# Kernel optimization log

Hardware: AMD Instinct MI355X
Metric: run time of the kernel (lower is better)

The kernel has to match this reference:

```python
import jax, jax.numpy as jnp
import numpy as np
from jax import lax

B, DIM, F, H, W = 2, 256, 4, 16, 16
HEADS, DIM_HEAD, GROUPS = 8, 64, 4
INNER = HEADS * DIM_HEAD            # 512
OFF_DIMS = INNER // GROUPS          # 128
CPB_DIM = DIM // 4                  # 64
DS = (2, 2, 2)                      # downsample_factor
OFFSET_SCALE = (2.0, 2.0, 2.0)


def norm_coords(coords, sizes):
    # coords: (..., 3) in (f, h, w) index units -> normalized to [-1, 1]
    s = jnp.array([max(sizes[0] - 1, 1), max(sizes[1] - 1, 1), max(sizes[2] - 1, 1)], dtype=coords.dtype)
    return 2.0 * coords / s - 1.0


def grid_sample_3d(vol, grid):
    # Faithful to F.grid_sample(..., mode='bilinear', padding_mode='zeros', align_corners=False)
    # vol: (N, C, D, H, W); grid: (N, P, 3) with last dim (x, y, z) -> (W, H, D) axes
    N, C, D, Hh, Ww = vol.shape
    P = grid.shape[1]
    ix = ((grid[..., 0] + 1.0) * Ww - 1.0) * 0.5
    iy = ((grid[..., 1] + 1.0) * Hh - 1.0) * 0.5
    iz = ((grid[..., 2] + 1.0) * D - 1.0) * 0.5
    x0, y0, z0 = jnp.floor(ix), jnp.floor(iy), jnp.floor(iz)
    tx, ty, tz = ix - x0, iy - y0, iz - z0
    vol_flat = vol.reshape(N, C, D * Hh * Ww)
    out = jnp.zeros((N, C, P), vol.dtype)
    for dz in (0, 1):
        for dy in (0, 1):
            for dx in (0, 1):
                xc, yc, zc = x0 + dx, y0 + dy, z0 + dz
                wgt = (jnp.where(dx, tx, 1.0 - tx) * jnp.where(dy, ty, 1.0 - ty) * jnp.where(dz, tz, 1.0 - tz))
                valid = ((xc >= 0) & (xc < Ww) & (yc >= 0) & (yc < Hh) & (zc >= 0) & (zc < D))
                xi = jnp.clip(xc, 0, Ww - 1).astype(jnp.int32)
                yi = jnp.clip(yc, 0, Hh - 1).astype(jnp.int32)
                zi = jnp.clip(zc, 0, D - 1).astype(jnp.int32)
                idx = (zi * Hh + yi) * Ww + xi                      # (N, P)
                vals = jnp.take_along_axis(vol_flat, jnp.broadcast_to(idx[:, None, :], (N, C, P)), axis=2)
                out = out + vals * (wgt * valid)[:, None, :]
    return out


def setup_inputs():
    key = jax.random.key(0)
    ks = jax.random.split(key, 16)
    r = lambda i, shape: jax.random.normal(ks[i], shape, dtype=jnp.float32) * 0.05
    return {
        'x': jax.random.normal(ks[0], (B, DIM, F, H, W), dtype=jnp.float32),
        'wq': r(1, (GROUPS, OFF_DIMS, DIM // GROUPS)),
        'wk': r(2, (GROUPS, OFF_DIMS, DIM // GROUPS)),
        'wv': r(3, (GROUPS, OFF_DIMS, DIM // GROUPS)),
        'off_dw_w': r(4, (OFF_DIMS, 1, 4, 4, 4)),
        'off_dw_b': r(5, (OFF_DIMS,)),
        'off_pw_w': r(6, (3, OFF_DIMS)),
        'cpb_w0': r(7, (3, CPB_DIM)),
        'cpb_b0': r(8, (CPB_DIM,)),
        'cpb_w1': r(9, (CPB_DIM, CPB_DIM)),
        'cpb_b1': r(10, (CPB_DIM,)),
        'cpb_w2': r(11, (CPB_DIM, HEADS // GROUPS)),
        'cpb_b2': r(12, (HEADS // GROUPS,)),
        'wo': r(13, (DIM, INNER)),
        'bo': r(14, (DIM,)),
    }


def reference(x, wq, wk, wv, off_dw_w, off_dw_b, off_pw_w, cpb_w0, cpb_b0, cpb_w1, cpb_b1, cpb_w2, cpb_b2, wo, bo):
    b = x.shape[0]
    f, h, w = x.shape[-3:]
    Pq = f * h * w
    scale = DIM_HEAD ** -0.5

    # grouped 1x1 conv to queries: channels are (g, d_out) ordered
    xg = x.reshape(b, GROUPS, DIM // GROUPS, Pq)
    q = jnp.einsum('bgip,goi->bgop', xg, wq)                        # (b, G, 128, Pq)

    # learned offsets: depthwise strided conv -> GELU -> 1x1 -> tanh -> scale
    gq = q.reshape(b * GROUPS, OFF_DIMS, f, h, w)
    off = lax.conv_general_dilated(gq, off_dw_w, window_strides=DS, padding=[(1, 1)] * 3,
                                   dimension_numbers=('NCDHW', 'OIDHW', 'NCDHW'),
                                   feature_group_count=OFF_DIMS)
    off = jax.nn.gelu(off + off_dw_b[None, :, None, None, None], approximate=False)
    off = jnp.einsum('ncdhw,oc->nodhw', off, off_pw_w)              # (bG, 3, fd, hd, wd)
    off = jnp.tanh(off) * jnp.array(OFFSET_SCALE, off.dtype)[None, :, None, None, None]

    fd, hd, wd = off.shape[-3:]
    Pj = fd * hd * wd
    base = jnp.stack(jnp.meshgrid(jnp.arange(fd), jnp.arange(hd), jnp.arange(wd), indexing='ij'), axis=0).astype(off.dtype)
    vgrid = base[None] + off
    vgrid_scaled = norm_coords(jnp.moveaxis(vgrid, 1, -1), (fd, hd, wd))  # (bG, fd, hd, wd, 3)
    grid_kv = vgrid_scaled.reshape(b * GROUPS, Pj, 3)

    # irregular gather of grouped features at deformed locations
    kv = grid_sample_3d(x.reshape(b * GROUPS, DIM // GROUPS, f, h, w), grid_kv)  # (bG, 64, Pj)
    kvg = kv.reshape(b, GROUPS, DIM // GROUPS, Pj)
    k = jnp.einsum('bgip,goi->bgop', kvg, wk)
    v = jnp.einsum('bgip,goi->bgop', kvg, wv)

    qh = (q * scale).reshape(b, HEADS, DIM_HEAD, Pq)
    kh = k.reshape(b, HEADS, DIM_HEAD, Pj)
    vh = v.reshape(b, HEADS, DIM_HEAD, Pj)
    sim = jnp.einsum('bhdi,bhdj->bhij', qh, kh)                     # (b, H, Pq, Pj)

    # CPB relative-position bias over (log-signed) pairwise grid differences
    baseq = jnp.stack(jnp.meshgrid(jnp.arange(f), jnp.arange(h), jnp.arange(w), indexing='ij'), axis=-1).astype(x.dtype)
    grid_q = norm_coords(baseq, (f, h, w)).reshape(Pq, 3)
    pos = grid_q[None, :, None, :] - grid_kv[:, None, :, :]         # (bG, Pq, Pj, 3)
    bias = jnp.sign(pos) * jnp.log1p(jnp.abs(pos))
    bias = jax.nn.relu(bias @ cpb_w0 + cpb_b0)
    bias = jax.nn.relu(bias @ cpb_w1 + cpb_b1)
    bias = bias @ cpb_w2 + cpb_b2                                   # (bG, Pq, Pj, H//G)
    bias = bias.reshape(b, GROUPS, Pq, Pj, HEADS // GROUPS)
    bias = jnp.transpose(bias, (0, 1, 4, 2, 3)).reshape(b, HEADS, Pq, Pj)

    attn = jax.nn.softmax(sim + bias, axis=-1)
    out = jnp.einsum('bhij,bhdj->bhdi', attn, vh).reshape(b, INNER, Pq)
    out = jnp.einsum('bcp,oc->bop', out, wo) + bo[None, :, None]
    return out.reshape(b, DIM, f, h, w)
```

## Files before the change

### kernel.cpp

```cpp
#include <hip/hip_runtime.h>
#include <hip/hip_bf16.h>
#include <hip/hip_fp16.h>
#include <math.h>

#define BB 2
#define DIMC 256
#define FF 4
#define HH 16
#define WW 16
#define GRP 4
#define CPG 64
#define ODIM 128
#define PQ 1024
#define PJ 128
#define NBG 8
#define INNERC 512

typedef _Float16 f16x8 __attribute__((ext_vector_type(8)));
typedef _Float16 f16x2 __attribute__((ext_vector_type(2)));
typedef float f32x4 __attribute__((ext_vector_type(4)));
typedef float f32x2 __attribute__((ext_vector_type(2)));

__global__ __launch_bounds__(512) void k_qdw(
    const float* __restrict__ x, const float* __restrict__ wq,
    const float* __restrict__ dww, const float* __restrict__ dwb,
    float* __restrict__ q, float* __restrict__ act) {
    __shared__ float qs[1024 * 4];
    int og = blockIdx.x & 31, bg = blockIdx.x >> 5;
    int b = bg >> 2, g = bg & 3;
    int o0 = og * 4;
    int tid = threadIdx.x;
    const float* xp = x + (size_t)(b * DIMC + g * CPG) * PQ;
    const float* wp = wq + (size_t)(g * ODIM + o0) * CPG;

    float accq[2][4] = {};
    #pragma unroll 8
    for (int i = 0; i < CPG; ++i) {
        float wv[4];
        #pragma unroll
        for (int k = 0; k < 4; ++k) wv[k] = wp[k * CPG + i];
        #pragma unroll
        for (int pi = 0; pi < 2; ++pi) {
            float xv = xp[(size_t)i * PQ + tid + pi * 512];
            #pragma unroll
            for (int k = 0; k < 4; ++k) accq[pi][k] += xv * wv[k];
        }
    }
    #pragma unroll
    for (int pi = 0; pi < 2; ++pi) {
        int p = tid + pi * 512;
        *(float4*)&qs[p * 4] = make_float4(accq[pi][0], accq[pi][1], accq[pi][2], accq[pi][3]);
        #pragma unroll
        for (int k = 0; k < 4; ++k)
            q[(size_t)(bg * ODIM + o0 + k) * PQ + p] = accq[pi][k];
    }
    __syncthreads();

    {
        int cl = tid & 3, j = tid >> 2;
        int c = o0 + cl;
        int xo = j & 7, yo = (j >> 3) & 7, zo = j >> 6;
        const float* wd = dww + c * 64;
        float acc = dwb[c];
        #pragma unroll
        for (int kz = 0; kz < 4; ++kz) {
            int z = 2 * zo - 1 + kz;
            if (z < 0 || z >= FF) continue;
            #pragma unroll
            for (int ky = 0; ky < 4; ++ky) {
                int y = 2 * yo - 1 + ky;
                if (y < 0 || y >= HH) continue;
                #pragma unroll
                for (int kx = 0; kx < 4; ++kx) {
                    int xx = 2 * xo - 1 + kx;
                    if (xx < 0 || xx >= WW) continue;
                    acc += qs[((z * HH + y) * WW + xx) * 4 + cl] * wd[(kz * 4 + ky) * 4 + kx];
                }
            }
        }
        act[((size_t)bg * PJ + j) * ODIM + c] =
            0.5f * acc * (1.0f + erff(acc * 0.70710678118654752f));
    }
}

__global__ __launch_bounds__(256) void k_kvf(
    const float* __restrict__ act, const float* __restrict__ pw,
    const float* __restrict__ x, const float* __restrict__ wk,
    const float* __restrict__ wv, float* __restrict__ gkv,
    _Float16* __restrict__ khT, _Float16* __restrict__ vhT) {
    __shared__ float red2[2][6];
    __shared__ float crd[2][3];
    __shared__ float kvs[2][64];
    int blk = blockIdx.x;
    int jt = blk & 63, bg = blk >> 6;
    int b = bg >> 2, g = bg & 3;
    int tid = threadIdx.x;
    int half = tid >> 7;
    int t = tid & 127;
    int j = jt * 2 + half;
    int wv_ = t >> 6;

    float val = act[((size_t)bg * PJ + j) * ODIM + t];
    float s0 = val * pw[t];
    float s1 = val * pw[ODIM + t];
    float s2 = val * pw[2 * ODIM + t];
    #pragma unroll
    for (int off = 32; off; off >>= 1) {
        s0 += __shfl_xor(s0, off);
        s1 += __shfl_xor(s1, off);
        s2 += __shfl_xor(s2, off);
    }
    if ((t & 63) == 0) {
        red2[half][wv_ * 3] = s0; red2[half][wv_ * 3 + 1] = s1; red2[half][wv_ * 3 + 2] = s2;
    }
    __syncthreads();
    if (t == 0) {
        s0 = red2[half][0] + red2[half][3];
        s1 = red2[half][1] + red2[half][4];
        s2 = red2[half][2] + red2[half][5];
        float xo = (float)(j & 7), yo = (float)((j >> 3) & 7), zo = (float)(j >> 6);
        float vf = zo + 2.f * tanhf(s0);
        float vh = yo + 2.f * tanhf(s1);
        float vw = xo + 2.f * tanhf(s2);
        float c0 = 2.f * vf - 1.f;
        float c1 = 2.f * vh / 7.f - 1.f;
        float c2 = 2.f * vw / 7.f - 1.f;
        crd[half][0] = c0; crd[half][1] = c1; crd[half][2] = c2;
        gkv[(bg * PJ + j) * 3 + 0] = c0;
        gkv[(bg * PJ + j) * 3 + 1] = c1;
        gkv[(bg * PJ + j) * 3 + 2] = c2;
    }
    __syncthreads();

    if (t < 64) {
        float ix = ((crd[half][0] + 1.f) * WW - 1.f) * 0.5f;
        float iy = ((crd[half][1] + 1.f) * HH - 1.f) * 0.5f;
        float iz = ((crd[half][2] + 1.f) * FF - 1.f) * 0.5f;
        float x0f = floorf(ix), y0f = floorf(iy), z0f = floorf(iz);
        float tx = ix - x0f, ty = iy - y0f, tz = iz - z0f;
        int x0 = (int)x0f, y0 = (int)y0f, z0 = (int)z0f;
        const float* vol = x + (size_t)(b * DIMC + g * CPG + t) * PQ;
        float acc = 0.f;
        #pragma unroll
        for (int dz = 0; dz < 2; ++dz) {
            int zc = z0 + dz;
            if (zc < 0 || zc >= FF) continue;
            float wz = dz ? tz : 1.f - tz;
            #pragma unroll
            for (int dy = 0; dy < 2; ++dy) {
                int yc = y0 + dy;
                if (yc < 0 || yc >= HH) continue;
                float wy = dy ? ty : 1.f - ty;
                #pragma unroll
                for (int dx = 0; dx < 2; ++dx) {
                    int xc = x0 + dx;
                    if (xc < 0 || xc >= WW) continue;
                    float wgt = wz * wy * (dx ? tx : 1.f - tx);
                    acc += vol[(zc * HH + yc) * WW + xc] * wgt;
                }
            }
        }
        kvs[half][t] = acc;
    }
    __syncthreads();

    const float* wkp = wk + (size_t)(g * ODIM + t) * CPG;
    const float* wvp = wv + (size_t)(g * ODIM + t) * CPG;
    float ak = 0.f, av = 0.f;
    #pragma unroll
    for (int i = 0; i < 64; i += 4) {
        float4 kv4 = *(const float4*)&kvs[half][i];
        float4 wk4 = *(const float4*)&wkp[i];
        float4 wv4 = *(const float4*)&wvp[i];
        ak += kv4.x * wk4.x + kv4.y * wk4.y + kv4.z * wk4.z + kv4.w * wk4.w;
        av += kv4.x * wv4.x + kv4.y * wv4.y + kv4.z * wv4.z + kv4.w * wv4.w;
    }
    {
        _Float16 khi = (_Float16)ak;
        khT[((size_t)(bg * 128 + j) * 2 + 0) * 128 + t] = khi;
        khT[((size_t)(bg * 128 + j) * 2 + 1) * 128 + t] = (_Float16)(ak - (float)khi);
        _Float16 vhi = (_Float16)av;
        vhT[((size_t)(bg * 128 + t) * 2 + 0) * 128 + j] = vhi;
        vhT[((size_t)(bg * 128 + t) * 2 + 1) * 128 + j] = (_Float16)(av - (float)vhi);
    }
}

__global__ __launch_bounds__(256) void k_cpa(
    const float* __restrict__ q, const _Float16* __restrict__ khT,
    const _Float16* __restrict__ vhT, const float* __restrict__ gkv,
    const float* __restrict__ w0, const float* __restrict__ b0,
    const float* __restrict__ w1, const float* __restrict__ b1,
    const float* __restrict__ w2, const float* __restrict__ b2,
    float* __restrict__ outh) {
    __shared__ __align__(16) float tbuf[4 * 2176];
    __shared__ __align__(16) float biasL[2 * 16 * 132];
    __shared__ float smax[64];
    __shared__ float ssum[64];

    int blk = blockIdx.x;
    int it = blk & 63, bg = blk >> 6;
    int b = bg >> 2, g = bg & 3;
    int tid = threadIdx.x;
    int w = tid >> 6, lane = tid & 63, col = lane & 15, quad = lane >> 4;

    uint4 bfr[2][4];
    #pragma unroll
    for (int kc = 0; kc < 2; ++kc)
        #pragma unroll
        for (int nt = 0; nt < 4; ++nt) {
            int n = nt * 16 + col;
            int kbase = kc * 32 + quad * 8;
            unsigned int pk[4];
            #pragma unroll
            for (int p = 0; p < 4; ++p) {
                f16x2 hv = {(_Float16)w1[(kbase + 2 * p) * 64 + n],
                            (_Float16)w1[(kbase + 2 * p + 1) * 64 + n]};
                pk[p] = *(unsigned int*)&hv;
            }
            bfr[kc][nt] = make_uint4(pk[0], pk[1], pk[2], pk[3]);
        }

    f16x2 w0a[2][4], w0b[2][4], w0c[2][4], b0h[2][4];
    #pragma unroll
    for (int kc = 0; kc < 2; ++kc) {
        int d0 = kc * 32 + quad * 8;
        #pragma unroll
        for (int pr = 0; pr < 4; ++pr) {
            w0a[kc][pr] = (f16x2){(_Float16)w0[d0 + 2 * pr], (_Float16)w0[d0 + 2 * pr + 1]};
            w0b[kc][pr] = (f16x2){(_Float16)w0[64 + d0 + 2 * pr], (_Float16)w0[64 + d0 + 2 * pr + 1]};
            w0c[kc][pr] = (f16x2){(_Float16)w0[128 + d0 + 2 * pr], (_Float16)w0[128 + d0 + 2 * pr + 1]};
            b0h[kc][pr] = (f16x2){(_Float16)b0[d0 + 2 * pr], (_Float16)b0[d0 + 2 * pr + 1]};
        }
    }
    f16x2 zero2 = {(_Float16)0.f, (_Float16)0.f};

    float g0r[8], g1r[8], g2r[8];
    #pragma unroll
    for (int mtg = 0; mtg < 8; ++mtg) {
        int jr = mtg * 16 + col;
        g0r[mtg] = gkv[(bg * PJ + jr) * 3 + 0];
        g1r[mtg] = gkv[(bg * PJ + jr) * 3 + 1];
        g2r[mtg] = gkv[(bg * PJ + jr) * 3 + 2];
    }
    float b1v[4]; f32x2 w2v[4];
    #pragma unroll
    for (int nt = 0; nt < 4; ++nt) {
        int jj = nt * 16 + col;
        b1v[nt] = b1[jj];
        w2v[nt] = *(const f32x2*)&w2[jj * 2];
    }
    f32x2 bias_b2 = *(const f32x2*)b2;
    f32x2* mytb = (f32x2*)&tbuf[w * 2176];

    #pragma unroll 1
    for (int ii = 0; ii < 4; ++ii) {
        int il = w * 4 + ii;
        int i = it * 16 + il;
        int wq_ = i & 15, hq = (i >> 4) & 15, fq = i >> 8;
        float cq0 = 2.f * fq / 3.f - 1.f;
        float cq1 = 2.f * hq / 15.f - 1.f;
        float cq2 = 2.f * wq_ / 15.f - 1.f;

        #pragma unroll 1
        for (int mh = 0; mh < 2; ++mh) {
            f16x2 t0h[4], t1h[4], t2h[4];
            #pragma unroll
            for (int mt = 0; mt < 4; ++mt) {
                int mtg = mh * 4 + mt;
                float p0 = cq0 - g0r[mtg];
                float p1 = cq1 - g1r[mtg];
                float p2 = cq2 - g2r[mtg];
                float t0 = copysignf(__logf(1.f + fabsf(p0)), p0);
                float t1 = copysignf(__logf(1.f + fabsf(p1)), p1);
                float t2 = copysignf(__logf(1.f + fabsf(p2)), p2);
                _Float16 h0 = (_Float16)t0, h1 = (_Float16)t1, h2 = (_Float16)t2;
                t0h[mt] = (f16x2){h0, h0};
                t1h[mt] = (f16x2){h1, h1};
                t2h[mt] = (f16x2){h2, h2};
            }
            f32x4 acc[4][4] = {};
            #pragma unroll
            for (int kc = 0; kc < 2; ++kc) {
                #pragma unroll
                for (int mt = 0; mt < 4; ++mt) {
                    unsigned int pk[4];
                    #pragma unroll
                    for (int pr = 0; pr < 4; ++pr) {
                        f16x2 z = b0h[kc][pr];
                        z += t0h[mt] * w0a[kc][pr];
                        z += t1h[mt] * w0b[kc][pr];
                        z += t2h[mt] * w0c[kc][pr];
                        z = __builtin_elementwise_max(z, zero2);
                        pk[pr] = *(unsigned int*)&z;
                    }
                    uint4 afu = make_uint4(pk[0], pk[1], pk[2], pk[3]);
                    f16x8 af = *(f16x8*)&afu;
                    #pragma unroll
                    for (int nt = 0; nt < 4; ++nt)
                        acc[mt][nt] = __builtin_amdgcn_mfma_f32_16x16x32_f16(
                            af, *(f16x8*)&bfr[kc][nt], acc[mt][nt], 0, 0, 0);
                }
            }
            #pragma unroll
            for (int mt = 0; mt < 4; ++mt)
                #pragma unroll
                for (int reg = 0; reg < 4; ++reg) {
                    f32x2 pp = {0.f, 0.f};
                    #pragma unroll
                    for (int nt = 0; nt < 4; ++nt) {
                        float hv = fmaxf(acc[mt][nt][reg] + b1v[nt], 0.f);
                        pp += hv * w2v[nt];
                    }
                    mytb[(mt * 16 + quad * 4 + reg) * 17 + col] = pp;
                }
            f32x2 s = bias_b2;
            {
                const f32x2* pr2 = mytb + lane * 17;
                #pragma unroll
                for (int c = 0; c < 16; ++c) s += pr2[c];
            }
            int jl = mh * 64 + lane;
            biasL[il * 132 + jl] = s.x;
            biasL[(16 + il) * 132 + jl] = s.y;
        }
    }
    __syncthreads();

    _Float16* attFh = (_Float16*)tbuf;
    _Float16* attFl = attFh + 4352;
    _Float16* qsFh  = attFh + 8704;
    _Float16* qsFl  = attFh + 10880;

    {
        int o = tid & 127, hf = tid >> 7;
        const float* qp = q + (size_t)(bg * ODIM + o) * PQ + it * 16 + hf * 8;
        float4 qa = *(const float4*)qp;
        float4 qb = *(const float4*)(qp + 4);
        float vals[8] = {qa.x, qa.y, qa.z, qa.w, qb.x, qb.y, qb.z, qb.w};
        #pragma unroll
        for (int k = 0; k < 8; ++k) {
            float v = vals[k] * 0.125f;
            _Float16 vhi = (_Float16)v;
            qsFh[(hf * 8 + k) * 136 + o] = vhi;
            qsFl[(hf * 8 + k) * 136 + o] = (_Float16)(v - (float)vhi);
        }
    }
    __syncthreads();

    int h = w >> 1, jh = w & 1;

    f16x8 aqh[2], aql[2];
    #pragma unroll
    for (int kc = 0; kc < 2; ++kc) {
        aqh[kc] = *(f16x8*)&qsFh[col * 136 + h * 64 + kc * 32 + quad * 8];
        aql[kc] = *(f16x8*)&qsFl[col * 136 + h * 64 + kc * 32 + quad * 8];
    }
    f32x4 acc[4];
    #pragma unroll
    for (int jt = 0; jt < 4; ++jt) {
        int j0 = jh * 64 + jt * 16;
        #pragma unroll
        for (int r = 0; r < 4; ++r)
            acc[jt][r] = biasL[(h * 16 + quad * 4 + r) * 132 + j0 + col];
    }
    const _Float16* kbase = khT + (size_t)(bg * 128) * 256 + h * 64 + quad * 8;
    #pragma unroll
    for (int kc = 0; kc < 2; ++kc) {
        #pragma unroll
        for (int jt = 0; jt < 4; ++jt) {
            const _Float16* kp = kbase + (size_t)(jh * 64 + jt * 16 + col) * 256 + kc * 32;
            f16x8 bh = *(const f16x8*)kp;
            f16x8 bl = *(const f16x8*)(kp + 128);
            acc[jt] = __builtin_amdgcn_mfma_f32_16x16x32_f16(aqh[kc], bh, acc[jt], 0, 0, 0);
            acc[jt] = __builtin_amdgcn_mfma_f32_16x16x32_f16(aql[kc], bh, acc[jt], 0, 0, 0);
            acc[jt] = __builtin_amdgcn_mfma_f32_16x16x32_f16(aqh[kc], bl, acc[jt], 0, 0, 0);
        }
    }

    float mrow[4];
    #pragma unroll
    for (int r = 0; r < 4; ++r) {
        float m = fmaxf(fmaxf(acc[0][r], acc[1][r]), fmaxf(acc[2][r], acc[3][r]));
        #pragma unroll
        for (int off = 1; off <= 8; off <<= 1) m = fmaxf(m, __shfl_xor(m, off));
        mrow[r] = m;
    }
    if (col == 0) {
        #pragma unroll
        for (int r = 0; r < 4; ++r) smax[(h * 2 + jh) * 16 + quad * 4 + r] = mrow[r];
    }
    __syncthreads();
    #pragma unroll
    for (int r = 0; r < 4; ++r)
        mrow[r] = fmaxf(smax[(h * 2) * 16 + quad * 4 + r],
                        smax[(h * 2 + 1) * 16 + quad * 4 + r]);

    float lrow[4] = {0.f, 0.f, 0.f, 0.f};
    #pragma unroll
    for (int jt = 0; jt < 4; ++jt) {
        int j0 = jh * 64 + jt * 16;
        #pragma unroll
        for (int r = 0; r < 4; ++r) {
            float p = __expf(acc[jt][r] - mrow[r]);
            lrow[r] += p;
            _Float16 phi = (_Float16)p;
            attFh[(h * 16 + quad * 4 + r) * 136 + j0 + col] = phi;
            attFl[(h * 16 + quad * 4 + r) * 136 + j0 + col] = (_Float16)(p - (float)phi);
        }
    }
    #pragma unroll
    for (int r = 0; r < 4; ++r) {
        float l = lrow[r];
        #pragma unroll
        for (int off = 1; off <= 8; off <<= 1) l += __shfl_xor(l, off);
        lrow[r] = l;
    }
    if (col == 0) {
        #pragma unroll
        for (int r = 0; r < 4; ++r) ssum[(h * 2 + jh) * 16 + quad * 4 + r] = lrow[r];
    }
    __syncthreads();

    f16x8 pah[4], pal[4];
    #pragma unroll
    for (int kc = 0; kc < 4; ++kc) {
        pah[kc] = *(f16x8*)&attFh[(h * 16 + col) * 136 + kc * 32 + quad * 8];
        pal[kc] = *(f16x8*)&attFl[(h * 16 + col) * 136 + kc * 32 + quad * 8];
    }
    float rinv[4];
    #pragma unroll
    for (int r = 0; r < 4; ++r)
        rinv[r] = 1.f / (ssum[(h * 2) * 16 + quad * 4 + r] +
                         ssum[(h * 2 + 1) * 16 + quad * 4 + r]);

    f32x4 oacc[2] = {};
    int chl0 = jh * 32 + col;
    #pragma unroll
    for (int kc = 0; kc < 4; ++kc) {
        #pragma unroll
        for (int nt = 0; nt < 2; ++nt) {
            int chl = chl0 + nt * 16;
            const _Float16* vp = vhT + (size_t)(bg * 128 + h * 64 + chl) * 256 + kc * 32 + quad * 8;
            f16x8 vh8 = *(const f16x8*)vp;
            f16x8 vl8 = *(const f16x8*)(vp + 128);
            oacc[nt] = __builtin_amdgcn_mfma_f32_16x16x32_f16(pah[kc], vh8, oacc[nt], 0, 0, 0);
            oacc[nt] = __builtin_amdgcn_mfma_f32_16x16x32_f16(pal[kc], vh8, oacc[nt], 0, 0, 0);
            oacc[nt] = __builtin_amdgcn_mfma_f32_16x16x32_f16(pah[kc], vl8, oacc[nt], 0, 0, 0);
        }
    }
    #pragma unroll
    for (int nt = 0; nt < 2; ++nt) {
        int chl = chl0 + nt * 16;
        #pragma unroll
        for (int r = 0; r < 4; ++r)
            outh[((size_t)(b * PQ + it * 16 + quad * 4 + r)) * INNERC + g * 128 + h * 64 + chl] =
                oacc[nt][r] * rinv[r];
    }
}

__global__ __launch_bounds__(256) void k_out(
    const float* __restrict__ outh, const float* __restrict__ wo,
    const float* __restrict__ bo, float* __restrict__ out) {
    __shared__ float At[32][68];
    __shared__ float Bt[32][36];
    int blk = blockIdx.x;
    int nt = blk & 7, mt = blk >> 3;
    int m0 = mt * 64, o0 = nt * 32;
    int tid = threadIdx.x;
    int tm = tid >> 4, tn = tid & 15;
    int mloc = tm * 4, nloc = tn * 2;

    int ra = tid >> 2, ca = (tid & 3) * 8;
    int rb = tid >> 3, cb = (tid & 7) * 4;

    float4 pa0, pa1, pb;
    {
        const float* Ap = outh + (size_t)(m0 + ra) * INNERC + ca;
        pa0 = *(const float4*)Ap;
        pa1 = *(const float4*)(Ap + 4);
        pb = *(const float4*)(wo + (size_t)(o0 + rb) * INNERC + cb);
    }

    float acc[4][2] = {};
    for (int ch = 0; ch < 16; ++ch) {
        #pragma unroll
        for (int k = 0; k < 4; ++k) {
            At[ca + k][ra] = ((const float*)&pa0)[k];
            At[ca + 4 + k][ra] = ((const float*)&pa1)[k];
            Bt[cb + k][rb] = ((const float*)&pb)[k];
        }
        __syncthreads();
        if (ch < 15) {
            int c0 = (ch + 1) * 32;
            const float* Ap = outh + (size_t)(m0 + ra) * INNERC + c0 + ca;
            pa0 = *(const float4*)Ap;
            pa1 = *(const float4*)(Ap + 4);
            pb = *(const float4*)(wo + (size_t)(o0 + rb) * INNERC + c0 + cb);
        }
        #pragma unroll
        for (int kk = 0; kk < 32; ++kk) {
            float4 a4 = *(const float4*)&At[kk][mloc];
            float2 b2 = *(const float2*)&Bt[kk][nloc];
            #pragma unroll
            for (int i = 0; i < 4; ++i) {
                float av = ((const float*)&a4)[i];
                acc[i][0] += av * b2.x;
                acc[i][1] += av * b2.y;
            }
        }
        __syncthreads();
    }

    #pragma unroll
    for (int jn = 0; jn < 2; ++jn) {
        int o = o0 + nloc + jn;
        float bv = bo[o];
        #pragma unroll
        for (int i = 0; i < 4; ++i) {
            int m = m0 + mloc + i;
            int b = m >> 10, p = m & 1023;
            out[((size_t)(b * DIMC + o)) * PQ + p] = acc[i][jn] + bv;
        }
    }
}

extern "C" void kernel_launch(void* const* d_in, const int* in_sizes, int n_in,
                              void* d_out, int out_size, void* d_ws, size_t ws_size,
                              hipStream_t stream) {
    const float* x   = (const float*)d_in[0];
    const float* wq  = (const float*)d_in[1];
    const float* wk  = (const float*)d_in[2];
    const float* wv  = (const float*)d_in[3];
    const float* dww = (const float*)d_in[4];
    const float* dwb = (const float*)d_in[5];
    const float* pw  = (const float*)d_in[6];
    const float* w0  = (const float*)d_in[7];
    const float* b0  = (const float*)d_in[8];
    const float* w1  = (const float*)d_in[9];
    const float* b1  = (const float*)d_in[10];
    const float* w2  = (const float*)d_in[11];
    const float* b2  = (const float*)d_in[12];
    const float* wo  = (const float*)d_in[13];
    const float* bo  = (const float*)d_in[14];
    float* out = (float*)d_out;

    float* ws_f  = (float*)d_ws;
    float* q     = ws_f;
    float* act   = q + 1048576;
    float* gkv   = act + 131072;
    _Float16* khT = (_Float16*)(gkv + 3072);
    _Float16* vhT = (_Float16*)(gkv + 3072 + 131072);
    float* outh  = gkv + 3072 + 262144;

    k_qdw<<<256, 512, 0, stream>>>(x, wq, dww, dwb, q, act);
    k_kvf<<<512, 256, 0, stream>>>(act, pw, x, wk, wv, gkv, khT, vhT);
    k_cpa<<<512, 256, 0, stream>>>(q, khT, vhT, gkv, w0, b0, w1, b1, w2, b2, outh);
    k_out<<<256, 256, 0, stream>>>(outh, wo, bo, out);
}
```

Measured before the change: 158.0 us.

## Use split-fp16 MFMA for output projection and double k_cpa block threads

```diff
diff --git a/kernel.cpp b/kernel.cpp
--- a/kernel.cpp
+++ b/kernel.cpp
@@ -17,6 +17,7 @@
 #define INNERC 512
 
 typedef _Float16 f16x8 __attribute__((ext_vector_type(8)));
+typedef _Float16 f16x4 __attribute__((ext_vector_type(4)));
 typedef _Float16 f16x2 __attribute__((ext_vector_type(2)));
 typedef float f32x4 __attribute__((ext_vector_type(4)));
 typedef float f32x2 __attribute__((ext_vector_type(2)));
@@ -185,17 +186,17 @@
     }
 }
 
-__global__ __launch_bounds__(256) void k_cpa(
+__global__ __launch_bounds__(512) void k_cpa(
     const float* __restrict__ q, const _Float16* __restrict__ khT,
     const _Float16* __restrict__ vhT, const float* __restrict__ gkv,
     const float* __restrict__ w0, const float* __restrict__ b0,
     const float* __restrict__ w1, const float* __restrict__ b1,
     const float* __restrict__ w2, const float* __restrict__ b2,
-    float* __restrict__ outh) {
-    __shared__ __align__(16) float tbuf[4 * 2176];
+    _Float16* __restrict__ outhH, _Float16* __restrict__ outhL) {
+    __shared__ __align__(16) float ubuf[6528];
     __shared__ __align__(16) float biasL[2 * 16 * 132];
-    __shared__ float smax[64];
-    __shared__ float ssum[64];
+    __shared__ float smax[128];
+    __shared__ float ssum[128];
 
     int blk = blockIdx.x;
     int it = blk & 63, bg = blk >> 6;
@@ -250,11 +251,11 @@
         w2v[nt] = *(const f32x2*)&w2[jj * 2];
     }
     f32x2 bias_b2 = *(const f32x2*)b2;
-    f32x2* mytb = (f32x2*)&tbuf[w * 2176];
+    f32x2* mytb = (f32x2*)&ubuf[w * 544];
 
     #pragma unroll 1
-    for (int ii = 0; ii < 4; ++ii) {
-        int il = w * 4 + ii;
+    for (int ii = 0; ii < 2; ++ii) {
+        int il = w * 2 + ii;
         int i = it * 16 + il;
         int wq_ = i & 15, hq = (i >> 4) & 15, fq = i >> 8;
         float cq0 = 2.f * fq / 3.f - 1.f;
@@ -302,7 +303,7 @@
                 }
             }
             #pragma unroll
-            for (int mt = 0; mt < 4; ++mt)
+            for (int mt = 0; mt < 4; ++mt) {
                 #pragma unroll
                 for (int reg = 0; reg < 4; ++reg) {
                     f32x2 pp = {0.f, 0.f};
@@ -311,43 +312,45 @@
                         float hv = fmaxf(acc[mt][nt][reg] + b1v[nt], 0.f);
                         pp += hv * w2v[nt];
                     }
-                    mytb[(mt * 16 + quad * 4 + reg) * 17 + col] = pp;
+                    mytb[(quad * 4 + reg) * 17 + col] = pp;
                 }
-            f32x2 s = bias_b2;
-            {
-                const f32x2* pr2 = mytb + lane * 17;
-                #pragma unroll
-                for (int c = 0; c < 16; ++c) s += pr2[c];
+                f32x2 s = mytb[col * 17 + quad * 4 + 0];
+                s += mytb[col * 17 + quad * 4 + 1];
+                s += mytb[col * 17 + quad * 4 + 2];
+                s += mytb[col * 17 + quad * 4 + 3];
+                s.x += __shfl_xor(s.x, 16); s.y += __shfl_xor(s.y, 16);
+                s.x += __shfl_xor(s.x, 32); s.y += __shfl_xor(s.y, 32);
+                if (quad == 0) {
+                    int jl = mh * 64 + mt * 16 + col;
+                    biasL[il * 132 + jl] = s.x + bias_b2.x;
+                    biasL[(16 + il) * 132 + jl] = s.y + bias_b2.y;
+                }
             }
-            int jl = mh * 64 + lane;
-            biasL[il * 132 + jl] = s.x;
-            biasL[(16 + il) * 132 + jl] = s.y;
-        }
-    }
-    __syncthreads();
-
-    _Float16* attFh = (_Float16*)tbuf;
+        }
+    }
+    __syncthreads();
+
+    _Float16* attFh = (_Float16*)ubuf;
     _Float16* attFl = attFh + 4352;
     _Float16* qsFh  = attFh + 8704;
     _Float16* qsFl  = attFh + 10880;
 
     {
         int o = tid & 127, hf = tid >> 7;
-        const float* qp = q + (size_t)(bg * ODIM + o) * PQ + it * 16 + hf * 8;
+        const float* qp = q + (size_t)(bg * ODIM + o) * PQ + it * 16 + hf * 4;
         float4 qa = *(const float4*)qp;
-        float4 qb = *(const float4*)(qp + 4);
-        float vals[8] = {qa.x, qa.y, qa.z, qa.w, qb.x, qb.y, qb.z, qb.w};
-        #pragma unroll
-        for (int k = 0; k < 8; ++k) {
-            float v = vals[k] * 0.125f;
+        float vals[4] = {qa.x, qa.y, qa.z, qa.w};
+        #pragma unroll
+        for (int k2 = 0; k2 < 4; ++k2) {
+            float v = vals[k2] * 0.125f;
             _Float16 vhi = (_Float16)v;
-            qsFh[(hf * 8 + k) * 136 + o] = vhi;
-            qsFl[(hf * 8 + k) * 136 + o] = (_Float16)(v - (float)vhi);
-        }
-    }
-    __syncthreads();
-
-    int h = w >> 1, jh = w & 1;
+            qsFh[(hf * 4 + k2) * 136 + o] = vhi;
+            qsFl[(hf * 4 + k2) * 136 + o] = (_Float16)(v - (float)vhi);
+        }
+    }
+    __syncthreads();
+
+    int h = w >> 2, p4 = w & 3;
 
     f16x8 aqh[2], aql[2];
     #pragma unroll
@@ -355,20 +358,20 @@
         aqh[kc] = *(f16x8*)&qsFh[col * 136 + h * 64 + kc * 32 + quad * 8];
         aql[kc] = *(f16x8*)&qsFl[col * 136 + h * 64 + kc * 32 + quad * 8];
     }
-    f32x4 acc[4];
-    #pragma unroll
-    for (int jt = 0; jt < 4; ++jt) {
-        int j0 = jh * 64 + jt * 16;
+    f32x4 acc[2];
+    #pragma unroll
+    for (int jt = 0; jt < 2; ++jt) {
+        int j0 = p4 * 32 + jt * 16;
         #pragma unroll
         for (int r = 0; r < 4; ++r)
             acc[jt][r] = biasL[(h * 16 + quad * 4 + r) * 132 + j0 + col];
     }
-    const _Float16* kbase = khT + (size_t)(bg * 128) * 256 + h * 64 + quad * 8;
     #pragma unroll
     for (int kc = 0; kc < 2; ++kc) {
         #pragma unroll
-        for (int jt = 0; jt < 4; ++jt) {
-            const _Float16* kp = kbase + (size_t)(jh * 64 + jt * 16 + col) * 256 + kc * 32;
+        for (int jt = 0; jt < 2; ++jt) {
+            const _Float16* kp = khT + (size_t)(bg * 128 + p4 * 32 + jt * 16 + col) * 256
+                                 + h * 64 + kc * 32 + quad * 8;
             f16x8 bh = *(const f16x8*)kp;
             f16x8 bl = *(const f16x8*)(kp + 128);
             acc[jt] = __builtin_amdgcn_mfma_f32_16x16x32_f16(aqh[kc], bh, acc[jt], 0, 0, 0);
@@ -380,25 +383,29 @@
     float mrow[4];
     #pragma unroll
     for (int r = 0; r < 4; ++r) {
-        float m = fmaxf(fmaxf(acc[0][r], acc[1][r]), fmaxf(acc[2][r], acc[3][r]));
+        float m = fmaxf(acc[0][r], acc[1][r]);
         #pragma unroll
         for (int off = 1; off <= 8; off <<= 1) m = fmaxf(m, __shfl_xor(m, off));
         mrow[r] = m;
     }
     if (col == 0) {
         #pragma unroll
-        for (int r = 0; r < 4; ++r) smax[(h * 2 + jh) * 16 + quad * 4 + r] = mrow[r];
-    }
-    __syncthreads();
-    #pragma unroll
-    for (int r = 0; r < 4; ++r)
-        mrow[r] = fmaxf(smax[(h * 2) * 16 + quad * 4 + r],
-                        smax[(h * 2 + 1) * 16 + quad * 4 + r]);
+        for (int r = 0; r < 4; ++r) smax[(h * 4 + p4) * 16 + quad * 4 + r] = mrow[r];
+    }
+    __syncthreads();
+    #pragma unroll
+    for (int r = 0; r < 4; ++r) {
+        float m = smax[(h * 4 + 0) * 16 + quad * 4 + r];
+        m = fmaxf(m, smax[(h * 4 + 1) * 16 + quad * 4 + r]);
+        m = fmaxf(m, smax[(h * 4 + 2) * 16 + quad * 4 + r]);
+        m = fmaxf(m, smax[(h * 4 + 3) * 16 + quad * 4 + r]);
+        mrow[r] = m;
+    }
 
     float lrow[4] = {0.f, 0.f, 0.f, 0.f};
     #pragma unroll
-    for (int jt = 0; jt < 4; ++jt) {
-        int j0 = jh * 64 + jt * 16;
+    for (int jt = 0; jt < 2; ++jt) {
+        int j0 = p4 * 32 + jt * 16;
         #pragma unroll
         for (int r = 0; r < 4; ++r) {
             float p = __expf(acc[jt][r] - mrow[r]);
@@ -417,7 +424,7 @@
     }
     if (col == 0) {
         #pragma unroll
-        for (int r = 0; r < 4; ++r) ssum[(h * 2 + jh) * 16 + quad * 4 + r] = lrow[r];
+        for (int r = 0; r < 4; ++r) ssum[(h * 4 + p4) * 16 + quad * 4 + r] = lrow[r];
     }
     __syncthreads();
 
@@ -430,97 +437,84 @@
     float rinv[4];
     #pragma unroll
     for (int r = 0; r < 4; ++r)
-        rinv[r] = 1.f / (ssum[(h * 2) * 16 + quad * 4 + r] +
-                         ssum[(h * 2 + 1) * 16 + quad * 4 + r]);
+        rinv[r] = 1.f / (ssum[(h * 4 + 0) * 16 + quad * 4 + r] +
+                         ssum[(h * 4 + 1) * 16 + quad * 4 + r] +
+                         ssum[(h * 4 + 2) * 16 + quad * 4 + r] +
+                         ssum[(h * 4 + 3) * 16 + quad * 4 + r]);
+
+    f32x4 oacc = {};
+    int chl = p4 * 16 + col;
+    #pragma unroll
+    for (int kc = 0; kc < 4; ++kc) {
+        const _Float16* vp = vhT + (size_t)(bg * 128 + h * 64 + chl) * 256 + kc * 32 + quad * 8;
+        f16x8 vh8 = *(const f16x8*)vp;
+        f16x8 vl8 = *(const f16x8*)(vp + 128);
+        oacc = __builtin_amdgcn_mfma_f32_16x16x32_f16(pah[kc], vh8, oacc, 0, 0, 0);
+        oacc = __builtin_amdgcn_mfma_f32_16x16x32_f16(pal[kc], vh8, oacc, 0, 0, 0);
+        oacc = __builtin_amdgcn_mfma_f32_16x16x32_f16(pah[kc], vl8, oacc, 0, 0, 0);
+    }
+    #pragma unroll
+    for (int r = 0; r < 4; ++r) {
+        float val = oacc[r] * rinv[r];
+        size_t idx = ((size_t)(b * PQ + it * 16 + quad * 4 + r)) * INNERC + g * 128 + h * 64 + chl;
+        _Float16 vhi = (_Float16)val;
+        outhH[idx] = vhi;
+        outhL[idx] = (_Float16)(val - (float)vhi);
+    }
+}
+
+__global__ __launch_bounds__(256) void k_wcvt(
+    const float* __restrict__ wo, _Float16* __restrict__ woH, _Float16* __restrict__ woL) {
+    int i = (blockIdx.x * 256 + threadIdx.x) * 4;
+    float4 v = *(const float4*)&wo[i];
+    f16x4 hh, ll;
+    hh[0] = (_Float16)v.x; ll[0] = (_Float16)(v.x - (float)hh[0]);
+    hh[1] = (_Float16)v.y; ll[1] = (_Float16)(v.y - (float)hh[1]);
+    hh[2] = (_Float16)v.z; ll[2] = (_Float16)(v.z - (float)hh[2]);
+    hh[3] = (_Float16)v.w; ll[3] = (_Float16)(v.w - (float)hh[3]);
+    *(f16x4*)&woH[i] = hh;
+    *(f16x4*)&woL[i] = ll;
+}
+
+__global__ __launch_bounds__(256) void k_out(
+    const _Float16* __restrict__ outhH, const _Float16* __restrict__ outhL,
+    const _Float16* __restrict__ woH, const _Float16* __restrict__ woL,
+    const float* __restrict__ bo, float* __restrict__ out) {
+    int blk = blockIdx.x;
+    int ntb = blk & 7, mtb = blk >> 3;
+    int tid = threadIdx.x;
+    int w = tid >> 6, lane = tid & 63, col = lane & 15, quad = lane >> 4;
+    int m0 = mtb * 64 + w * 16;
+    int o0 = ntb * 32;
+
+    const _Float16* ahb = outhH + (size_t)(m0 + col) * INNERC + quad * 8;
+    const _Float16* alb = outhL + (size_t)(m0 + col) * INNERC + quad * 8;
 
     f32x4 oacc[2] = {};
-    int chl0 = jh * 32 + col;
-    #pragma unroll
-    for (int kc = 0; kc < 4; ++kc) {
+    #pragma unroll 4
+    for (int ks = 0; ks < 16; ++ks) {
+        f16x8 ah = *(const f16x8*)(ahb + ks * 32);
+        f16x8 al = *(const f16x8*)(alb + ks * 32);
         #pragma unroll
         for (int nt = 0; nt < 2; ++nt) {
-            int chl = chl0 + nt * 16;
-            const _Float16* vp = vhT + (size_t)(bg * 128 + h * 64 + chl) * 256 + kc * 32 + quad * 8;
-            f16x8 vh8 = *(const f16x8*)vp;
-            f16x8 vl8 = *(const f16x8*)(vp + 128);
-            oacc[nt] = __builtin_amdgcn_mfma_f32_16x16x32_f16(pah[kc], vh8, oacc[nt], 0, 0, 0);
-            oacc[nt] = __builtin_amdgcn_mfma_f32_16x16x32_f16(pal[kc], vh8, oacc[nt], 0, 0, 0);
-            oacc[nt] = __builtin_amdgcn_mfma_f32_16x16x32_f16(pah[kc], vl8, oacc[nt], 0, 0, 0);
+            const _Float16* bp = woH + (size_t)(o0 + nt * 16 + col) * INNERC + ks * 32 + quad * 8;
+            const _Float16* lp = woL + (size_t)(o0 + nt * 16 + col) * INNERC + ks * 32 + quad * 8;
+            f16x8 bh = *(const f16x8*)bp;
+            f16x8 bl = *(const f16x8*)lp;
+            oacc[nt] = __builtin_amdgcn_mfma_f32_16x16x32_f16(ah, bh, oacc[nt], 0, 0, 0);
+            oacc[nt] = __builtin_amdgcn_mfma_f32_16x16x32_f16(al, bh, oacc[nt], 0, 0, 0);
+            oacc[nt] = __builtin_amdgcn_mfma_f32_16x16x32_f16(ah, bl, oacc[nt], 0, 0, 0);
         }
     }
     #pragma unroll
     for (int nt = 0; nt < 2; ++nt) {
-        int chl = chl0 + nt * 16;
-        #pragma unroll
-        for (int r = 0; r < 4; ++r)
-            outh[((size_t)(b * PQ + it * 16 + quad * 4 + r)) * INNERC + g * 128 + h * 64 + chl] =
-                oacc[nt][r] * rinv[r];
-    }
-}
-
-__global__ __launch_bounds__(256) void k_out(
-    const float* __restrict__ outh, const float* __restrict__ wo,
-    const float* __restrict__ bo, float* __restrict__ out) {
-    __shared__ float At[32][68];
-    __shared__ float Bt[32][36];
-    int blk = blockIdx.x;
-    int nt = blk & 7, mt = blk >> 3;
-    int m0 = mt * 64, o0 = nt * 32;
-    int tid = threadIdx.x;
-    int tm = tid >> 4, tn = tid & 15;
-    int mloc = tm * 4, nloc = tn * 2;
-
-    int ra = tid >> 2, ca = (tid & 3) * 8;
-    int rb = tid >> 3, cb = (tid & 7) * 4;
-
-    float4 pa0, pa1, pb;
-    {
-        const float* Ap = outh + (size_t)(m0 + ra) * INNERC + ca;
-        pa0 = *(const float4*)Ap;
-        pa1 = *(const float4*)(Ap + 4);
-        pb = *(const float4*)(wo + (size_t)(o0 + rb) * INNERC + cb);
-    }
-
-    float acc[4][2] = {};
-    for (int ch = 0; ch < 16; ++ch) {
-        #pragma unroll
-        for (int k = 0; k < 4; ++k) {
-            At[ca + k][ra] = ((const float*)&pa0)[k];
-            At[ca + 4 + k][ra] = ((const float*)&pa1)[k];
-            Bt[cb + k][rb] = ((const float*)&pb)[k];
-        }
-        __syncthreads();
-        if (ch < 15) {
-            int c0 = (ch + 1) * 32;
-            const float* Ap = outh + (size_t)(m0 + ra) * INNERC + c0 + ca;
-            pa0 = *(const float4*)Ap;
-            pa1 = *(const float4*)(Ap + 4);
-            pb = *(const float4*)(wo + (size_t)(o0 + rb) * INNERC + c0 + cb);
-        }
-        #pragma unroll
-        for (int kk = 0; kk < 32; ++kk) {
-            float4 a4 = *(const float4*)&At[kk][mloc];
-            float2 b2 = *(const float2*)&Bt[kk][nloc];
-            #pragma unroll
-            for (int i = 0; i < 4; ++i) {
-                float av = ((const float*)&a4)[i];
-                acc[i][0] += av * b2.x;
-                acc[i][1] += av * b2.y;
-            }
-        }
-        __syncthreads();
-    }
-
-    #pragma unroll
-    for (int jn = 0; jn < 2; ++jn) {
-        int o = o0 + nloc + jn;
+        int o = o0 + nt * 16 + col;
         float bv = bo[o];
-        #pragma unroll
-        for (int i = 0; i < 4; ++i) {
-            int m = m0 + mloc + i;
-            int b = m >> 10, p = m & 1023;
-            out[((size_t)(b * DIMC + o)) * PQ + p] = acc[i][jn] + bv;
-        }
+        int m = m0 + quad * 4;
+        int bb = m >> 10, p = m & 1023;
+        float4 st = make_float4(oacc[nt][0] + bv, oacc[nt][1] + bv,
+                                oacc[nt][2] + bv, oacc[nt][3] + bv);
+        *(float4*)&out[((size_t)(bb * DIMC + o)) * PQ + p] = st;
     }
 }
 
@@ -548,12 +542,16 @@
     float* q     = ws_f;
     float* act   = q + 1048576;
     float* gkv   = act + 131072;
-    _Float16* khT = (_Float16*)(gkv + 3072);
-    _Float16* vhT = (_Float16*)(gkv + 3072 + 131072);
-    float* outh  = gkv + 3072 + 262144;
-
+    _Float16* khT   = (_Float16*)(gkv + 3072);
+    _Float16* vhT   = khT + 262144;
+    _Float16* outhH = vhT + 262144;
+    _Float16* outhL = outhH + 1048576;
+    _Float16* woH   = outhL + 1048576;
+    _Float16* woL   = woH + 131072;
+
+    k_wcvt<<<128, 256, 0, stream>>>(wo, woH, woL);
     k_qdw<<<256, 512, 0, stream>>>(x, wq, dww, dwb, q, act);
     k_kvf<<<512, 256, 0, stream>>>(act, pw, x, wk, wv, gkv, khT, vhT);
-    k_cpa<<<512, 256, 0, stream>>>(q, khT, vhT, gkv, w0, b0, w1, b1, w2, b2, outh);
-    k_out<<<256, 256, 0, stream>>>(outh, wo, bo, out);
+    k_cpa<<<512, 512, 0, stream>>>(q, khT, vhT, gkv, w0, b0, w1, b1, w2, b2, outhH, outhL);
+    k_out<<<256, 256, 0, stream>>>(outhH, outhL, woH, woL, bo, out);
 }
```

Measured after the change: 164.7 us. 4.2% more time.

## Split bias MLP into its own kernel and move output projection to split-fp16 MFMA

Applied to the files above, without the earlier changes.

```diff
diff --git a/kernel.cpp b/kernel.cpp
--- a/kernel.cpp
+++ b/kernel.cpp
@@ -17,6 +17,7 @@
 #define INNERC 512
 
 typedef _Float16 f16x8 __attribute__((ext_vector_type(8)));
+typedef _Float16 f16x4 __attribute__((ext_vector_type(4)));
 typedef _Float16 f16x2 __attribute__((ext_vector_type(2)));
 typedef float f32x4 __attribute__((ext_vector_type(4)));
 typedef float f32x2 __attribute__((ext_vector_type(2)));
@@ -24,12 +25,22 @@
 __global__ __launch_bounds__(512) void k_qdw(
     const float* __restrict__ x, const float* __restrict__ wq,
     const float* __restrict__ dww, const float* __restrict__ dwb,
+    const float* __restrict__ wo, _Float16* __restrict__ woH, _Float16* __restrict__ woL,
     float* __restrict__ q, float* __restrict__ act) {
     __shared__ float qs[1024 * 4];
     int og = blockIdx.x & 31, bg = blockIdx.x >> 5;
     int b = bg >> 2, g = bg & 3;
     int o0 = og * 4;
     int tid = threadIdx.x;
+
+    {
+        int i = blockIdx.x * 512 + tid;
+        float v = wo[i];
+        _Float16 hh = (_Float16)v;
+        woH[i] = hh;
+        woL[i] = (_Float16)(v - (float)hh);
+    }
+
     const float* xp = x + (size_t)(b * DIMC + g * CPG) * PQ;
     const float* wp = wq + (size_t)(g * ODIM + o0) * CPG;
 
@@ -185,21 +196,15 @@
     }
 }
 
-__global__ __launch_bounds__(256) void k_cpa(
-    const float* __restrict__ q, const _Float16* __restrict__ khT,
-    const _Float16* __restrict__ vhT, const float* __restrict__ gkv,
+__global__ __launch_bounds__(256, 4) void k_bias(
+    const float* __restrict__ gkv,
     const float* __restrict__ w0, const float* __restrict__ b0,
     const float* __restrict__ w1, const float* __restrict__ b1,
     const float* __restrict__ w2, const float* __restrict__ b2,
-    float* __restrict__ outh) {
+    float* __restrict__ biasG) {
     __shared__ __align__(16) float tbuf[4 * 2176];
-    __shared__ __align__(16) float biasL[2 * 16 * 132];
-    __shared__ float smax[64];
-    __shared__ float ssum[64];
-
     int blk = blockIdx.x;
-    int it = blk & 63, bg = blk >> 6;
-    int b = bg >> 2, g = bg & 3;
+    int mh = blk & 1, it = (blk >> 1) & 63, bg = blk >> 7;
     int tid = threadIdx.x;
     int w = tid >> 6, lane = tid & 63, col = lane & 15, quad = lane >> 4;
 
@@ -234,13 +239,13 @@
     }
     f16x2 zero2 = {(_Float16)0.f, (_Float16)0.f};
 
-    float g0r[8], g1r[8], g2r[8];
-    #pragma unroll
-    for (int mtg = 0; mtg < 8; ++mtg) {
-        int jr = mtg * 16 + col;
-        g0r[mtg] = gkv[(bg * PJ + jr) * 3 + 0];
-        g1r[mtg] = gkv[(bg * PJ + jr) * 3 + 1];
-        g2r[mtg] = gkv[(bg * PJ + jr) * 3 + 2];
+    float g0r[4], g1r[4], g2r[4];
+    #pragma unroll
+    for (int mt = 0; mt < 4; ++mt) {
+        int jr = (mh * 4 + mt) * 16 + col;
+        g0r[mt] = gkv[(bg * PJ + jr) * 3 + 0];
+        g1r[mt] = gkv[(bg * PJ + jr) * 3 + 1];
+        g2r[mt] = gkv[(bg * PJ + jr) * 3 + 2];
     }
     float b1v[4]; f32x2 w2v[4];
     #pragma unroll
@@ -251,6 +256,7 @@
     }
     f32x2 bias_b2 = *(const f32x2*)b2;
     f32x2* mytb = (f32x2*)&tbuf[w * 2176];
+    float* bb = biasG + (size_t)((bg * 64 + it) * 2) * 2048;
 
     #pragma unroll 1
     for (int ii = 0; ii < 4; ++ii) {
@@ -261,75 +267,83 @@
         float cq1 = 2.f * hq / 15.f - 1.f;
         float cq2 = 2.f * wq_ / 15.f - 1.f;
 
-        #pragma unroll 1
-        for (int mh = 0; mh < 2; ++mh) {
-            f16x2 t0h[4], t1h[4], t2h[4];
+        f16x2 t0h[4], t1h[4], t2h[4];
+        #pragma unroll
+        for (int mt = 0; mt < 4; ++mt) {
+            float p0 = cq0 - g0r[mt];
+            float p1 = cq1 - g1r[mt];
+            float p2 = cq2 - g2r[mt];
+            float t0 = copysignf(__logf(1.f + fabsf(p0)), p0);
+            float t1 = copysignf(__logf(1.f + fabsf(p1)), p1);
+            float t2 = copysignf(__logf(1.f + fabsf(p2)), p2);
+            _Float16 h0 = (_Float16)t0, h1 = (_Float16)t1, h2 = (_Float16)t2;
+            t0h[mt] = (f16x2){h0, h0};
+            t1h[mt] = (f16x2){h1, h1};
+            t2h[mt] = (f16x2){h2, h2};
+        }
+        f32x4 acc[4][4] = {};
+        #pragma unroll
+        for (int kc = 0; kc < 2; ++kc) {
             #pragma unroll
             for (int mt = 0; mt < 4; ++mt) {
-                int mtg = mh * 4 + mt;
-                float p0 = cq0 - g0r[mtg];
-                float p1 = cq1 - g1r[mtg];
-                float p2 = cq2 - g2r[mtg];
-                float t0 = copysignf(__logf(1.f + fabsf(p0)), p0);
-                float t1 = copysignf(__logf(1.f + fabsf(p1)), p1);
-                float t2 = copysignf(__logf(1.f + fabsf(p2)), p2);
-                _Float16 h0 = (_Float16)t0, h1 = (_Float16)t1, h2 = (_Float16)t2;
-                t0h[mt] = (f16x2){h0, h0};
-                t1h[mt] = (f16x2){h1, h1};
-                t2h[mt] = (f16x2){h2, h2};
+                unsigned int pk[4];
+                #pragma unroll
+                for (int pr = 0; pr < 4; ++pr) {
+                    f16x2 z = b0h[kc][pr];
+                    z += t0h[mt] * w0a[kc][pr];
+                    z += t1h[mt] * w0b[kc][pr];
+                    z += t2h[mt] * w0c[kc][pr];
+                    z = __builtin_elementwise_max(z, zero2);
+                    pk[pr] = *(unsigned int*)&z;
+                }
+                uint4 afu = make_uint4(pk[0], pk[1], pk[2], pk[3]);
+                f16x8 af = *(f16x8*)&afu;
+                #pragma unroll
+                for (int nt = 0; nt < 4; ++nt)
+                    acc[mt][nt] = __builtin_amdgcn_mfma_f32_16x16x32_f16(
+                        af, *(f16x8*)&bfr[kc][nt], acc[mt][nt], 0, 0, 0);
             }
-            f32x4 acc[4][4] = {};
-            #pragma unroll
-            for (int kc = 0; kc < 2; ++kc) {
+        }
+        #pragma unroll
+        for (int mt = 0; mt < 4; ++mt)
+            #pragma unroll
+            for (int reg = 0; reg < 4; ++reg) {
+                f32x2 pp = {0.f, 0.f};
                 #pragma unroll
-                for (int mt = 0; mt < 4; ++mt) {
-                    unsigned int pk[4];
-                    #pragma unroll
-                    for (int pr = 0; pr < 4; ++pr) {
-                        f16x2 z = b0h[kc][pr];
-                        z += t0h[mt] * w0a[kc][pr];
-                        z += t1h[mt] * w0b[kc][pr];
-                        z += t2h[mt] * w0c[kc][pr];
-                        z = __builtin_elementwise_max(z, zero2);
-                        pk[pr] = *(unsigned int*)&z;
-                    }
-                    uint4 afu = make_uint4(pk[0], pk[1], pk[2], pk[3]);
-                    f16x8 af = *(f16x8*)&afu;
-                    #pragma unroll
-                    for (int nt = 0; nt < 4; ++nt)
-                        acc[mt][nt] = __builtin_amdgcn_mfma_f32_16x16x32_f16(
-                            af, *(f16x8*)&bfr[kc][nt], acc[mt][nt], 0, 0, 0);
+                for (int nt = 0; nt < 4; ++nt) {
+                    float hv = fmaxf(acc[mt][nt][reg] + b1v[nt], 0.f);
+                    pp += hv * w2v[nt];
                 }
+                mytb[(mt * 16 + quad * 4 + reg) * 17 + col] = pp;
             }
-            #pragma unroll
-            for (int mt = 0; mt < 4; ++mt)
-                #pragma unroll
-                for (int reg = 0; reg < 4; ++reg) {
-                    f32x2 pp = {0.f, 0.f};
-                    #pragma unroll
-                    for (int nt = 0; nt < 4; ++nt) {
-                        float hv = fmaxf(acc[mt][nt][reg] + b1v[nt], 0.f);
-                        pp += hv * w2v[nt];
-                    }
-                    mytb[(mt * 16 + quad * 4 + reg) * 17 + col] = pp;
-                }
-            f32x2 s = bias_b2;
-            {
-                const f32x2* pr2 = mytb + lane * 17;
-                #pragma unroll
-                for (int c = 0; c < 16; ++c) s += pr2[c];
-            }
-            int jl = mh * 64 + lane;
-            biasL[il * 132 + jl] = s.x;
-            biasL[(16 + il) * 132 + jl] = s.y;
-        }
-    }
-    __syncthreads();
-
-    _Float16* attFh = (_Float16*)tbuf;
-    _Float16* attFl = attFh + 4352;
-    _Float16* qsFh  = attFh + 8704;
-    _Float16* qsFl  = attFh + 10880;
+        f32x2 s = bias_b2;
+        {
+            const f32x2* pr2 = mytb + lane * 17;
+            #pragma unroll
+            for (int c = 0; c < 16; ++c) s += pr2[c];
+        }
+        int jl = mh * 64 + lane;
+        bb[(size_t)il * 128 + jl] = s.x;
+        bb[(size_t)(16 + il) * 128 + jl] = s.y;
+    }
+}
+
+__global__ __launch_bounds__(256) void k_attn(
+    const float* __restrict__ q, const _Float16* __restrict__ khT,
+    const _Float16* __restrict__ vhT, const float* __restrict__ biasG,
+    _Float16* __restrict__ outhH, _Float16* __restrict__ outhL) {
+    __shared__ __align__(16) _Float16 attFh[2 * 16 * 136];
+    __shared__ __align__(16) _Float16 attFl[2 * 16 * 136];
+    __shared__ __align__(16) _Float16 qsFh[16 * 136];
+    __shared__ __align__(16) _Float16 qsFl[16 * 136];
+    __shared__ float smax[64];
+    __shared__ float ssum[64];
+
+    int blk = blockIdx.x;
+    int it = blk & 63, bg = blk >> 6;
+    int b = bg >> 2, g = bg & 3;
+    int tid = threadIdx.x;
+    int w = tid >> 6, lane = tid & 63, col = lane & 15, quad = lane >> 4;
 
     {
         int o = tid & 127, hf = tid >> 7;
@@ -355,13 +369,14 @@
         aqh[kc] = *(f16x8*)&qsFh[col * 136 + h * 64 + kc * 32 + quad * 8];
         aql[kc] = *(f16x8*)&qsFl[col * 136 + h * 64 + kc * 32 + quad * 8];
     }
+    const float* bbase = biasG + (size_t)((bg * 64 + it) * 2 + h) * 2048;
     f32x4 acc[4];
     #pragma unroll
     for (int jt = 0; jt < 4; ++jt) {
         int j0 = jh * 64 + jt * 16;
         #pragma unroll
         for (int r = 0; r < 4; ++r)
-            acc[jt][r] = biasL[(h * 16 + quad * 4 + r) * 132 + j0 + col];
+            acc[jt][r] = bbase[(size_t)(quad * 4 + r) * 128 + j0 + col];
     }
     const _Float16* kbase = khT + (size_t)(bg * 128) * 256 + h * 64 + quad * 8;
     #pragma unroll
@@ -452,75 +467,56 @@
     for (int nt = 0; nt < 2; ++nt) {
         int chl = chl0 + nt * 16;
         #pragma unroll
-        for (int r = 0; r < 4; ++r)
-            outh[((size_t)(b * PQ + it * 16 + quad * 4 + r)) * INNERC + g * 128 + h * 64 + chl] =
-                oacc[nt][r] * rinv[r];
+        for (int r = 0; r < 4; ++r) {
+            float val = oacc[nt][r] * rinv[r];
+            size_t idx = ((size_t)(b * PQ + it * 16 + quad * 4 + r)) * INNERC
+                         + g * 128 + h * 64 + chl;
+            _Float16 vhi = (_Float16)val;
+            outhH[idx] = vhi;
+            outhL[idx] = (_Float16)(val - (float)vhi);
+        }
     }
 }
 
 __global__ __launch_bounds__(256) void k_out(
-    const float* __restrict__ outh, const float* __restrict__ wo,
+    const _Float16* __restrict__ outhH, const _Float16* __restrict__ outhL,
+    const _Float16* __restrict__ woH, const _Float16* __restrict__ woL,
     const float* __restrict__ bo, float* __restrict__ out) {
-    __shared__ float At[32][68];
-    __shared__ float Bt[32][36];
     int blk = blockIdx.x;
-    int nt = blk & 7, mt = blk >> 3;
-    int m0 = mt * 64, o0 = nt * 32;
+    int ntb = blk & 7, mtb = blk >> 3;
     int tid = threadIdx.x;
-    int tm = tid >> 4, tn = tid & 15;
-    int mloc = tm * 4, nloc = tn * 2;
-
-    int ra = tid >> 2, ca = (tid & 3) * 8;
-    int rb = tid >> 3, cb = (tid & 7) * 4;
-
-    float4 pa0, pa1, pb;
-    {
-        const float* Ap = outh + (size_t)(m0 + ra) * INNERC + ca;
-        pa0 = *(const float4*)Ap;
-        pa1 = *(const float4*)(Ap + 4);
-        pb = *(const float4*)(wo + (size_t)(o0 + rb) * INNERC + cb);
-    }
-
-    float acc[4][2] = {};
-    for (int ch = 0; ch < 16; ++ch) {
-        #pragma unroll
-        for (int k = 0; k < 4; ++k) {
-            At[ca + k][ra] = ((const float*)&pa0)[k];
-            At[ca + 4 + k][ra] = ((const float*)&pa1)[k];
-            Bt[cb + k][rb] = ((const float*)&pb)[k];
-        }
-        __syncthreads();
-        if (ch < 15) {
-            int c0 = (ch + 1) * 32;
-            const float* Ap = outh + (size_t)(m0 + ra) * INNERC + c0 + ca;
-            pa0 = *(const float4*)Ap;
-            pa1 = *(const float4*)(Ap + 4);
-            pb = *(const float4*)(wo + (size_t)(o0 + rb) * INNERC + c0 + cb);
-        }
-        #pragma unroll
-        for (int kk = 0; kk < 32; ++kk) {
-            float4 a4 = *(const float4*)&At[kk][mloc];
-            float2 b2 = *(const float2*)&Bt[kk][nloc];
-            #pragma unroll
-            for (int i = 0; i < 4; ++i) {
-                float av = ((const float*)&a4)[i];
-                acc[i][0] += av * b2.x;
-                acc[i][1] += av * b2.y;
-            }
-        }
-        __syncthreads();
-    }
-
-    #pragma unroll
-    for (int jn = 0; jn < 2; ++jn) {
-        int o = o0 + nloc + jn;
+    int w = tid >> 6, lane = tid & 63, col = lane & 15, quad = lane >> 4;
+    int m0 = mtb * 64 + w * 16;
+    int o0 = ntb * 32;
+
+    const _Float16* ahb = outhH + (size_t)(m0 + col) * INNERC + quad * 8;
+    const _Float16* alb = outhL + (size_t)(m0 + col) * INNERC + quad * 8;
+
+    f32x4 oacc[2] = {};
+    #pragma unroll 4
+    for (int ks = 0; ks < 16; ++ks) {
+        f16x8 ah = *(const f16x8*)(ahb + ks * 32);
+        f16x8 al = *(const f16x8*)(alb + ks * 32);
+        #pragma unroll
+        for (int nt = 0; nt < 2; ++nt) {
+            const _Float16* bp = woH + (size_t)(o0 + nt * 16 + col) * INNERC + ks * 32 + quad * 8;
+            const _Float16* lp = woL + (size_t)(o0 + nt * 16 + col) * INNERC + ks * 32 + quad * 8;
+            f16x8 bh = *(const f16x8*)bp;
+            f16x8 bl = *(const f16x8*)lp;
+            oacc[nt] = __builtin_amdgcn_mfma_f32_16x16x32_f16(ah, bh, oacc[nt], 0, 0, 0);
+            oacc[nt] = __builtin_amdgcn_mfma_f32_16x16x32_f16(al, bh, oacc[nt], 0, 0, 0);
+            oacc[nt] = __builtin_amdgcn_mfma_f32_16x16x32_f16(ah, bl, oacc[nt], 0, 0, 0);
+        }
+    }
+    #pragma unroll
+    for (int nt = 0; nt < 2; ++nt) {
+        int o = o0 + nt * 16 + col;
         float bv = bo[o];
-        #pragma unroll
-        for (int i = 0; i < 4; ++i) {
-            int m = m0 + mloc + i;
-            int b = m >> 10, p = m & 1023;
-            out[((size_t)(b * DIMC + o)) * PQ + p] = acc[i][jn] + bv;
-        }
+        int m = m0 + quad * 4;
+        int bb = m >> 10, p = m & 1023;
+        float4 st = make_float4(oacc[nt][0] + bv, oacc[nt][1] + bv,
+                                oacc[nt][2] + bv, oacc[nt][3] + bv);
+        *(float4*)&out[((size_t)(bb * DIMC + o)) * PQ + p] = st;
     }
 }
 
@@ -548,12 +544,17 @@
     float* q     = ws_f;
     float* act   = q + 1048576;
     float* gkv   = act + 131072;
-    _Float16* khT = (_Float16*)(gkv + 3072);
-    _Float16* vhT = (_Float16*)(gkv + 3072 + 131072);
-    float* outh  = gkv + 3072 + 262144;
-
-    k_qdw<<<256, 512, 0, stream>>>(x, wq, dww, dwb, q, act);
+    _Float16* khT   = (_Float16*)(gkv + 3072);
+    _Float16* vhT   = khT + 262144;
+    _Float16* outhH = vhT + 262144;
+    _Float16* outhL = outhH + 1048576;
+    _Float16* woH   = outhL + 1048576;
+    _Float16* woL   = woH + 131072;
+    float* biasG = (float*)(woL + 131072);
+
+    k_qdw<<<256, 512, 0, stream>>>(x, wq, dww, dwb, wo, woH, woL, q, act);
     k_kvf<<<512, 256, 0, stream>>>(act, pw, x, wk, wv, gkv, khT, vhT);
-    k_cpa<<<512, 256, 0, stream>>>(q, khT, vhT, gkv, w0, b0, w1, b1, w2, b2, outh);
-    k_out<<<256, 256, 0, stream>>>(outh, wo, bo, out);
+    k_bias<<<1024, 256, 0, stream>>>(gkv, w0, b0, w1, b1, w2, b2, biasG);
+    k_attn<<<512, 256, 0, stream>>>(q, khT, vhT, biasG, outhH, outhL);
+    k_out<<<256, 256, 0, stream>>>(outhH, outhL, woH, woL, bo, out);
 }
```

New measurement: 207.0 us. 1.31x slower.
